# Kernel optimization log

Hardware: AMD Instinct MI355X
Metric: run time of the kernel (lower is better)

## Reference

```python
import jax, jax.numpy as jnp
import numpy as np

TOP_K = 2  # config.moe_config.top_k


def setup_inputs() -> dict:
    key = jax.random.key(0)
    k0, k1, k2, k3 = jax.random.split(key, 4)
    T, H, I, E = 8192, 2048, 1408, 8  # tokens, hidden, moe_intermediate, experts
    x = jax.random.normal(k0, (T, H), jnp.float32)
    router_weight = jax.random.normal(k1, (E, H), jnp.float32) * 0.02
    gate_up_proj = jax.random.normal(k2, (E, H, 2 * I), jnp.float32) * 0.02
    down_proj = jax.random.normal(k3, (E, I, H), jnp.float32) * 0.02
    return {"x": x, "router_weight": router_weight,
            "gate_up_proj": gate_up_proj, "down_proj": down_proj}


def _moe_forward(x, router_weight, gate_up_proj, down_proj):
    # Router: fp32 gating linear (no bias), softmax over experts, top-k,
    # then scatter the top-k softmax weights into a dense [T, E] gate tensor
    # (topk_version=False path of Router.top_k_softmax).
    T = x.shape[0]
    E = router_weight.shape[0]
    logits = x.astype(jnp.float32) @ router_weight.T            # [T, E]
    probs = jax.nn.softmax(logits, axis=-1)                      # [T, E]
    topk_w, topk_idx = jax.lax.top_k(probs, TOP_K)               # [T, k]
    gates = jnp.zeros_like(logits).at[
        jnp.arange(T)[:, None], topk_idx].set(topk_w)            # [T, E] sparse gates

    # Grouped expert MLP (GroupedMLP): merged gate/up GEMM, SwiGLU, down GEMM.
    # Dispatch/permute + grouped GEMM + weighted combine is mathematically
    # out[t] = sum_e gates[t, e] * MLP_e(x[t]); expressed here as a fixed loop
    # over the small expert set with masked accumulation (jit-friendly).
    out = jnp.zeros_like(x)
    for e in range(E):
        gu = x @ gate_up_proj[e]                                 # [T, 2I]
        g, u = jnp.split(gu, 2, axis=-1)
        h = (jax.nn.silu(g) * u) @ down_proj[e]                  # [T, H]
        out = out + gates[:, e:e + 1].astype(x.dtype) * h
    return out


def reference(x, router_weight, gate_up_proj, down_proj):
    return _moe_forward(x, router_weight, gate_up_proj, down_proj)
```

## Files before the change

### kernel.cpp

```cpp
#include <hip/hip_runtime.h>
#include <hip/hip_bf16.h>
#include <cstdint>
#include <cstddef>

#define T_TOK 8192
#define H_DIM 2048
#define I_DIM 1408
#define E_NUM 8
#define BM 128
#define BK 64
#define ROWS_CAP (2 * T_TOK + E_NUM * BM)
#define MAX_MT (ROWS_CAP / BM)
#define NT1 (I_DIM / 64)
#define NT2 (H_DIM / 128)

typedef __attribute__((ext_vector_type(8))) short short8;
typedef __attribute__((ext_vector_type(4))) float f32x4;
typedef __attribute__((ext_vector_type(8))) unsigned short bf16x8;
typedef __attribute__((ext_vector_type(4))) unsigned short bf16x4;
typedef __attribute__((ext_vector_type(8))) _Float16 h16x8;

static __device__ __forceinline__ unsigned short f2bf(float f) {
  unsigned u = __float_as_uint(f);
  u += 0x7FFFu + ((u >> 16) & 1u);
  return (unsigned short)(u >> 16);
}

static __device__ __forceinline__ void gld_lds16(const void* g, void* l) {
  __builtin_amdgcn_global_load_lds(
      (__attribute__((address_space(1))) unsigned int*)g,
      (__attribute__((address_space(3))) unsigned int*)l, 16, 0, 0);
}

static __device__ __forceinline__ void remap_tile(int bid, int nb, int nt_cols,
                                                  int& m_t, int& n_t) {
  int chunk = nb >> 3;
  int wg = (bid & 7) * chunk + (bid >> 3);
  int grp = wg / (nt_cols * 4);
  int rem = wg % (nt_cols * 4);
  n_t = rem >> 2;
  m_t = grp * 4 + (rem & 3);
}

__global__ __launch_bounds__(256) void router_kernel(
    const float* __restrict__ x, const float* __restrict__ rw,
    int* __restrict__ topk_idx, float* __restrict__ topk_w, int* __restrict__ meta) {
  int t = blockIdx.x * 4 + (threadIdx.x >> 6);
  int lane = threadIdx.x & 63;
  const float* xr = x + (size_t)t * H_DIM;
  float acc[E_NUM];
#pragma unroll
  for (int e = 0; e < E_NUM; e++) acc[e] = 0.f;
  for (int j = lane; j < H_DIM; j += 64) {
    float xv = xr[j];
#pragma unroll
    for (int e = 0; e < E_NUM; e++) acc[e] += xv * rw[e * H_DIM + j];
  }
#pragma unroll
  for (int e = 0; e < E_NUM; e++) {
    float v = acc[e];
#pragma unroll
    for (int s = 32; s > 0; s >>= 1) v += __shfl_xor(v, s);
    acc[e] = v;
  }
  if (lane == 0) {
    int i0 = 0;
#pragma unroll
    for (int e = 1; e < E_NUM; e++) if (acc[e] > acc[i0]) i0 = e;
    int i1 = (i0 == 0) ? 1 : 0;
#pragma unroll
    for (int e = 0; e < E_NUM; e++) if (e != i0 && acc[e] > acc[i1]) i1 = e;
    float mx = acc[0];
#pragma unroll
    for (int e = 1; e < E_NUM; e++) mx = fmaxf(mx, acc[e]);
    float sum = 0.f, p[E_NUM];
#pragma unroll
    for (int e = 0; e < E_NUM; e++) { p[e] = expf(acc[e] - mx); sum += p[e]; }
    float inv = 1.f / sum;
    topk_idx[t * 2] = i0;  topk_idx[t * 2 + 1] = i1;
    topk_w[t * 2] = p[i0] * inv;  topk_w[t * 2 + 1] = p[i1] * inv;
    atomicAdd(&meta[i0], 1);
    atomicAdd(&meta[i1], 1);
  }
}

__global__ void scan_kernel(int* __restrict__ meta, int* __restrict__ row_token) {
  __shared__ int s_off[E_NUM + 1];
  if (threadIdx.x == 0) {
    int o = 0, nt = 0;
    for (int e = 0; e < E_NUM; e++) {
      meta[16 + e] = o; s_off[e] = o;
      int c = meta[e];
      int mtc = (c + BM - 1) / BM;
      for (int m = 0; m < mtc; m++) { meta[64 + nt] = e; meta[256 + nt] = o + m * BM; nt++; }
      o += mtc * BM;
      meta[8 + e] = 0;
    }
    meta[16 + E_NUM] = o; s_off[E_NUM] = o;
    meta[32] = nt;
  }
  __syncthreads();
  for (int e = 0; e < E_NUM; e++) {
    int lo = s_off[e] + meta[e], hi = s_off[e + 1];
    for (int r = lo + (int)threadIdx.x; r < hi; r += 64) row_token[r] = -1;
  }
}

__global__ __launch_bounds__(256) void bucket_kernel(
    const int* __restrict__ topk_idx, int* __restrict__ meta,
    int* __restrict__ row_token, int* __restrict__ tok2row) {
  int i = blockIdx.x * 256 + threadIdx.x;
  if (i >= 2 * T_TOK) return;
  int e = topk_idx[i];
  int pos = atomicAdd(&meta[8 + e], 1);
  int r = meta[16 + e] + pos;
  row_token[r] = i >> 1;
  tok2row[i] = r;
}

__global__ __launch_bounds__(256) void cvt_kernel(const float* __restrict__ in,
                                                  unsigned short* __restrict__ out, int n) {
  int i = (blockIdx.x * 256 + threadIdx.x) * 8;
  if (i >= n) return;
  bf16x8 v;
#pragma unroll
  for (int j = 0; j < 8; j++) v[j] = f2bf(in[i + j]);
  *(bf16x8*)(out + i) = v;
}

__global__ __launch_bounds__(256) void tcvt_kernel(const float* __restrict__ in,
                                                   unsigned short* __restrict__ out,
                                                   int R, int C) {
  __shared__ unsigned short tile[64][66];
  size_t ebase = (size_t)blockIdx.z * (size_t)R * (size_t)C;
  const float* src = in + ebase;
  unsigned short* dst = out + ebase;
  int c0 = blockIdx.x * 64, r0 = blockIdx.y * 64;
  int tid = threadIdx.x;
  int q = tid & 15, s = tid >> 4;
#pragma unroll
  for (int it = 0; it < 4; it++) {
    int rr = it * 16 + s;
    f32x4 v = *(const f32x4*)(src + (size_t)(r0 + rr) * C + c0 + q * 4);
#pragma unroll
    for (int j = 0; j < 4; j++) tile[rr][q * 4 + j] = f2bf(v[j]);
  }
  __syncthreads();
#pragma unroll
  for (int it = 0; it < 4; it++) {
    int cc = it * 16 + s;
    bf16x4 v;
#pragma unroll
    for (int j = 0; j < 4; j++) v[j] = tile[q * 4 + j][cc];
    *(bf16x4*)(dst + (size_t)(c0 + cc) * R + r0 + q * 4) = v;
  }
}

__global__ __launch_bounds__(256) void gemm1_kernel(
    const unsigned short* __restrict__ xb,
    const unsigned short* __restrict__ wgu,
    unsigned short* __restrict__ hbuf,
    const int* __restrict__ row_token, const int* __restrict__ meta) {
  int m_t, n_t;
  remap_tile(blockIdx.x, NT1 * MAX_MT, NT1, m_t, n_t);
  if (m_t >= meta[32]) return;
  int e = meta[64 + m_t];
  int row0 = meta[256 + m_t];
  int n0h = n_t * 64;

  __shared__ alignas(16) char smem[65536];

  int tid = threadIdx.x, lane = tid & 63, wid = tid >> 6;
  const unsigned short* asrc[4];
  const unsigned short* bsrc[4];
  {
    const unsigned short* wb = wgu + (size_t)e * (2 * (size_t)I_DIM) * H_DIM;
#pragma unroll
    for (int i = 0; i < 4; i++) {
      int r = i * 32 + (tid >> 3);
      int ch = ((tid & 7) ^ (r & 7)) * 8;
      int tok = row_token[row0 + r];
      if (tok < 0) tok = 0;
      asrc[i] = xb + (size_t)tok * H_DIM + ch;
      int wr = (r < 64) ? (n0h + r) : (I_DIM + n0h + (r - 64));
      bsrc[i] = wb + (size_t)wr * H_DIM + ch;
    }
  }
  f32x4 acc[4][4] = {};
  int mrow = (wid >> 1) * 64 + (lane & 15);
  int brow = (wid & 1) * 64 + (lane & 15);

#define STAGE1(buf, kof_)                                                     \
  {                                                                           \
    int kof = (kof_);                                                         \
    char* b = smem + (buf) * 32768;                                           \
    _Pragma("unroll") for (int i = 0; i < 4; i++) {                           \
      gld_lds16(asrc[i] + kof, b + i * 4096 + wid * 1024);                    \
      gld_lds16(bsrc[i] + kof, b + 16384 + i * 4096 + wid * 1024);            \
    }                                                                         \
  }

  STAGE1(0, 0);
  __syncthreads();
  int cur = 0;
  for (int kt = 0; kt < H_DIM / BK; kt++) {
    if (kt + 1 < H_DIM / BK) STAGE1(cur ^ 1, (kt + 1) * BK);
    const unsigned short* sA = (const unsigned short*)(smem + cur * 32768);
    const unsigned short* sB = sA + 8192;
#pragma unroll
    for (int kk = 0; kk < 2; kk++) {
      int krd = ((kk * 4 + (lane >> 4)) ^ (lane & 7)) * 8;
      short8 af[4], bf[4];
#pragma unroll
      for (int f = 0; f < 4; f++) {
        af[f] = *(const short8*)(sA + (mrow + f * 16) * BK + krd);
        bf[f] = *(const short8*)(sB + (brow + f * 16) * BK + krd);
      }
#pragma unroll
      for (int fm = 0; fm < 4; fm++)
#pragma unroll
        for (int fn = 0; fn < 4; fn++)
          acc[fm][fn] = __builtin_amdgcn_mfma_f32_16x16x32_bf16(af[fm], bf[fn], acc[fm][fn], 0, 0, 0);
    }
    __syncthreads();
    cur ^= 1;
  }

  float* xw = (float*)smem + (wid >> 1) * 4096;
  if (wid & 1) {
#pragma unroll
    for (int fm = 0; fm < 4; fm++)
#pragma unroll
      for (int r = 0; r < 4; r++) {
        int mloc = fm * 16 + (lane >> 4) * 4 + r;
#pragma unroll
        for (int fn = 0; fn < 4; fn++)
          xw[mloc * 64 + fn * 16 + (lane & 15)] = acc[fm][fn][r];
      }
  }
  __syncthreads();
  if (!(wid & 1)) {
    int mbase = row0 + (wid >> 1) * 64;
#pragma unroll
    for (int fm = 0; fm < 4; fm++)
#pragma unroll
      for (int r = 0; r < 4; r++) {
        int mloc = fm * 16 + (lane >> 4) * 4 + r;
        size_t rbase = (size_t)(mbase + mloc) * I_DIM + n0h;
#pragma unroll
        for (int fn = 0; fn < 4; fn++) {
          float g = acc[fm][fn][r];
          float u = xw[mloc * 64 + fn * 16 + (lane & 15)];
          float hv = (g / (1.f + __expf(-g))) * u;
          hbuf[rbase + fn * 16 + (lane & 15)] = f2bf(hv);
        }
      }
  }
}

__global__ __launch_bounds__(256) void gemm2_kernel(
    const unsigned short* __restrict__ hbuf,
    const unsigned short* __restrict__ wd,
    _Float16* __restrict__ part,
    const int* __restrict__ meta) {
  int m_t, n_t;
  remap_tile(blockIdx.x, NT2 * MAX_MT, NT2, m_t, n_t);
  if (m_t >= meta[32]) return;
  int e = meta[64 + m_t];
  int row0 = meta[256 + m_t];
  int n0 = n_t * 128;

  __shared__ alignas(16) char smem[65536];

  int tid = threadIdx.x, lane = tid & 63, wid = tid >> 6;
  const unsigned short* asrc[4];
  const unsigned short* bsrc[4];
  {
    const unsigned short* wb = wd + (size_t)e * (size_t)H_DIM * I_DIM;
#pragma unroll
    for (int i = 0; i < 4; i++) {
      int r = i * 32 + (tid >> 3);
      int ch = ((tid & 7) ^ (r & 7)) * 8;
      asrc[i] = hbuf + (size_t)(row0 + r) * I_DIM + ch;
      bsrc[i] = wb + (size_t)(n0 + r) * I_DIM + ch;
    }
  }
  f32x4 acc[4][4] = {};
  int mrow = (wid >> 1) * 64 + (lane & 15);
  int brow = (wid & 1) * 64 + (lane & 15);

  STAGE1(0, 0);
  __syncthreads();
  int cur = 0;
  for (int kt = 0; kt < I_DIM / BK; kt++) {
    if (kt + 1 < I_DIM / BK) STAGE1(cur ^ 1, (kt + 1) * BK);
    const unsigned short* sA = (const unsigned short*)(smem + cur * 32768);
    const unsigned short* sB = sA + 8192;
#pragma unroll
    for (int kk = 0; kk < 2; kk++) {
      int krd = ((kk * 4 + (lane >> 4)) ^ (lane & 7)) * 8;
      short8 af[4], bf[4];
#pragma unroll
      for (int f = 0; f < 4; f++) {
        af[f] = *(const short8*)(sA + (mrow + f * 16) * BK + krd);
        bf[f] = *(const short8*)(sB + (brow + f * 16) * BK + krd);
      }
#pragma unroll
      for (int fm = 0; fm < 4; fm++)
#pragma unroll
        for (int fn = 0; fn < 4; fn++)
          acc[fm][fn] = __builtin_amdgcn_mfma_f32_16x16x32_bf16(af[fm], bf[fn], acc[fm][fn], 0, 0, 0);
    }
    __syncthreads();
    cur ^= 1;
  }
  int m0 = (wid >> 1) * 64;
  int nn0 = n0 + (wid & 1) * 64 + (lane & 15);
#pragma unroll
  for (int fm = 0; fm < 4; fm++)
#pragma unroll
    for (int r = 0; r < 4; r++) {
      int rr = row0 + m0 + fm * 16 + (lane >> 4) * 4 + r;
      _Float16* prow = part + (size_t)rr * H_DIM + nn0;
#pragma unroll
      for (int fn = 0; fn < 4; fn++)
        prow[fn * 16] = (_Float16)acc[fm][fn][r];
    }
}

__global__ __launch_bounds__(256) void combine_kernel(
    const _Float16* __restrict__ part, const int* __restrict__ tok2row,
    const float* __restrict__ topk_w, float* __restrict__ out) {
  int t = blockIdx.x;
  int c = threadIdx.x * 8;
  int r0 = tok2row[2 * t], r1 = tok2row[2 * t + 1];
  float w0 = topk_w[2 * t], w1 = topk_w[2 * t + 1];
  h16x8 p0 = *(const h16x8*)(part + (size_t)r0 * H_DIM + c);
  h16x8 p1 = *(const h16x8*)(part + (size_t)r1 * H_DIM + c);
  float* o = out + (size_t)t * H_DIM + c;
  f32x4 lo, hi;
#pragma unroll
  for (int j = 0; j < 4; j++) lo[j] = w0 * (float)p0[j] + w1 * (float)p1[j];
#pragma unroll
  for (int j = 0; j < 4; j++) hi[j] = w0 * (float)p0[4 + j] + w1 * (float)p1[4 + j];
  *(f32x4*)o = lo;
  *(f32x4*)(o + 4) = hi;
}

extern "C" void kernel_launch(void* const* d_in, const int* in_sizes, int n_in,
                              void* d_out, int out_size, void* d_ws, size_t ws_size,
                              hipStream_t stream) {
  const float* x   = (const float*)d_in[0];
  const float* rw  = (const float*)d_in[1];
  const float* wgu = (const float*)d_in[2];
  const float* wdn = (const float*)d_in[3];
  float* out = (float*)d_out;

  char* ws = (char*)d_ws;
  size_t off = 0;
  auto alloc = [&](size_t bytes) {
    void* p = ws + off;
    off += (bytes + 255) & ~(size_t)255;
    return p;
  };
  int* meta            = (int*)alloc(4096);
  int* topk_idx        = (int*)alloc((size_t)2 * T_TOK * 4);
  float* topk_w        = (float*)alloc((size_t)2 * T_TOK * 4);
  int* tok2row         = (int*)alloc((size_t)2 * T_TOK * 4);
  int* row_token       = (int*)alloc((size_t)ROWS_CAP * 4);
  unsigned short* xb    = (unsigned short*)alloc((size_t)T_TOK * H_DIM * 2);
  unsigned short* wgu_t = (unsigned short*)alloc((size_t)E_NUM * 2 * I_DIM * H_DIM * 2);
  unsigned short* wd_t  = (unsigned short*)alloc((size_t)E_NUM * H_DIM * I_DIM * 2);
  unsigned short* hbuf  = (unsigned short*)alloc((size_t)ROWS_CAP * I_DIM * 2);
  _Float16* part = (_Float16*)wgu_t;

  if (off > ws_size) {
    (void)hipMemsetAsync(d_out, 0, (size_t)out_size * sizeof(float), stream);
    return;
  }

  (void)hipMemsetAsync(meta, 0, 4096, stream);

  cvt_kernel<<<(T_TOK * H_DIM / 8 + 255) / 256, 256, 0, stream>>>(x, xb, T_TOK * H_DIM);
  tcvt_kernel<<<dim3(2 * I_DIM / 64, H_DIM / 64, E_NUM), 256, 0, stream>>>(wgu, wgu_t, H_DIM, 2 * I_DIM);
  tcvt_kernel<<<dim3(H_DIM / 64, I_DIM / 64, E_NUM), 256, 0, stream>>>(wdn, wd_t, I_DIM, H_DIM);

  router_kernel<<<T_TOK / 4, 256, 0, stream>>>(x, rw, topk_idx, topk_w, meta);
  scan_kernel<<<1, 64, 0, stream>>>(meta, row_token);
  bucket_kernel<<<(2 * T_TOK + 255) / 256, 256, 0, stream>>>(topk_idx, meta, row_token, tok2row);

  gemm1_kernel<<<NT1 * MAX_MT, 256, 0, stream>>>(xb, wgu_t, hbuf, row_token, meta);
  gemm2_kernel<<<NT2 * MAX_MT, 256, 0, stream>>>(hbuf, wd_t, part, meta);
  combine_kernel<<<T_TOK, 256, 0, stream>>>(part, tok2row, topk_w, out);
}
```

Measured before the change: 776.7 us.

## Fuse x bf16 conversion into router and merge weight transpose kernels

```diff
diff --git a/kernel.cpp b/kernel.cpp
--- a/kernel.cpp
+++ b/kernel.cpp
@@ -44,17 +44,26 @@
 
 __global__ __launch_bounds__(256) void router_kernel(
     const float* __restrict__ x, const float* __restrict__ rw,
+    unsigned short* __restrict__ xb,
     int* __restrict__ topk_idx, float* __restrict__ topk_w, int* __restrict__ meta) {
   int t = blockIdx.x * 4 + (threadIdx.x >> 6);
   int lane = threadIdx.x & 63;
   const float* xr = x + (size_t)t * H_DIM;
+  unsigned short* xbr = xb + (size_t)t * H_DIM;
   float acc[E_NUM];
 #pragma unroll
   for (int e = 0; e < E_NUM; e++) acc[e] = 0.f;
-  for (int j = lane; j < H_DIM; j += 64) {
-    float xv = xr[j];
-#pragma unroll
-    for (int e = 0; e < E_NUM; e++) acc[e] += xv * rw[e * H_DIM + j];
+  for (int j = lane * 4; j < H_DIM; j += 256) {
+    f32x4 v = *(const f32x4*)(xr + j);
+    bf16x4 b;
+#pragma unroll
+    for (int u = 0; u < 4; u++) b[u] = f2bf(v[u]);
+    *(bf16x4*)(xbr + j) = b;
+#pragma unroll
+    for (int e = 0; e < E_NUM; e++) {
+      f32x4 w = *(const f32x4*)(rw + e * H_DIM + j);
+      acc[e] += v[0] * w[0] + v[1] * w[1] + v[2] * w[2] + v[3] * w[3];
+    }
   }
 #pragma unroll
   for (int e = 0; e < E_NUM; e++) {
@@ -118,24 +127,21 @@
   tok2row[i] = r;
 }
 
-__global__ __launch_bounds__(256) void cvt_kernel(const float* __restrict__ in,
-                                                  unsigned short* __restrict__ out, int n) {
-  int i = (blockIdx.x * 256 + threadIdx.x) * 8;
-  if (i >= n) return;
-  bf16x8 v;
-#pragma unroll
-  for (int j = 0; j < 8; j++) v[j] = f2bf(in[i + j]);
-  *(bf16x8*)(out + i) = v;
-}
-
-__global__ __launch_bounds__(256) void tcvt_kernel(const float* __restrict__ in,
-                                                   unsigned short* __restrict__ out,
-                                                   int R, int C) {
-  __shared__ unsigned short tile[64][66];
-  size_t ebase = (size_t)blockIdx.z * (size_t)R * (size_t)C;
-  const float* src = in + ebase;
-  unsigned short* dst = out + ebase;
+__global__ __launch_bounds__(256) void tcvt2_kernel(
+    const float* __restrict__ wgu, const float* __restrict__ wdn,
+    unsigned short* __restrict__ wgu_t, unsigned short* __restrict__ wd_t) {
+  __shared__ unsigned short st[64][66];
+  int z = blockIdx.z;
+  const float* src; unsigned short* dst; int R, C;
+  if (z < E_NUM) {
+    R = H_DIM; C = 2 * I_DIM;
+    src = wgu + (size_t)z * R * C;  dst = wgu_t + (size_t)z * R * C;
+  } else {
+    R = I_DIM; C = H_DIM;
+    src = wdn + (size_t)(z - E_NUM) * R * C;  dst = wd_t + (size_t)(z - E_NUM) * R * C;
+  }
   int c0 = blockIdx.x * 64, r0 = blockIdx.y * 64;
+  if (c0 >= C || r0 >= R) return;
   int tid = threadIdx.x;
   int q = tid & 15, s = tid >> 4;
 #pragma unroll
@@ -143,16 +149,17 @@
     int rr = it * 16 + s;
     f32x4 v = *(const f32x4*)(src + (size_t)(r0 + rr) * C + c0 + q * 4);
 #pragma unroll
-    for (int j = 0; j < 4; j++) tile[rr][q * 4 + j] = f2bf(v[j]);
+    for (int j = 0; j < 4; j++) st[rr][q * 4 + j] = f2bf(v[j]);
   }
   __syncthreads();
-#pragma unroll
-  for (int it = 0; it < 4; it++) {
-    int cc = it * 16 + s;
-    bf16x4 v;
-#pragma unroll
-    for (int j = 0; j < 4; j++) v[j] = tile[q * 4 + j][cc];
-    *(bf16x4*)(dst + (size_t)(c0 + cc) * R + r0 + q * 4) = v;
+  int cc = tid >> 3, rseg = (tid & 7) * 8;
+#pragma unroll
+  for (int it = 0; it < 2; it++) {
+    int c = it * 32 + cc;
+    bf16x8 v;
+#pragma unroll
+    for (int k = 0; k < 8; k++) v[k] = st[rseg + k][c];
+    *(bf16x8*)(dst + (size_t)(c0 + c) * R + r0 + rseg) = v;
   }
 }
 
@@ -381,11 +388,9 @@
 
   (void)hipMemsetAsync(meta, 0, 4096, stream);
 
-  cvt_kernel<<<(T_TOK * H_DIM / 8 + 255) / 256, 256, 0, stream>>>(x, xb, T_TOK * H_DIM);
-  tcvt_kernel<<<dim3(2 * I_DIM / 64, H_DIM / 64, E_NUM), 256, 0, stream>>>(wgu, wgu_t, H_DIM, 2 * I_DIM);
-  tcvt_kernel<<<dim3(H_DIM / 64, I_DIM / 64, E_NUM), 256, 0, stream>>>(wdn, wd_t, I_DIM, H_DIM);
-
-  router_kernel<<<T_TOK / 4, 256, 0, stream>>>(x, rw, topk_idx, topk_w, meta);
+  tcvt2_kernel<<<dim3(2 * I_DIM / 64, H_DIM / 64, 2 * E_NUM), 256, 0, stream>>>(wgu, wdn, wgu_t, wd_t);
+
+  router_kernel<<<T_TOK / 4, 256, 0, stream>>>(x, rw, xb, topk_idx, topk_w, meta);
   scan_kernel<<<1, 64, 0, stream>>>(meta, row_token);
   bucket_kernel<<<(2 * T_TOK + 255) / 256, 256, 0, stream>>>(topk_idx, meta, row_token, tok2row);
 
```

After: 757.6 us. 2.5% less time.
